# Kernel tuning notes

Hardware: AMD Instinct MI355X
Metric: run time of the kernel (lower is better)

The kernel has to match this reference:

```python
import jax, jax.numpy as jnp
import numpy as np

EPS = 1e-5


def _dwconv(x, w, pad):
    # x: [N,C,H,W]; w: [C,1,k,k] depthwise kernel (groups = C)
    return jax.lax.conv_general_dilated(
        x, w, window_strides=(1, 1), padding=[(pad, pad), (pad, pad)],
        feature_group_count=w.shape[0],
        dimension_numbers=("NCHW", "OIHW", "NCHW"))


def _bn(y, g, b, m, v):
    # inference-mode BatchNorm2d using running stats; per-channel affine
    scale = (g / jnp.sqrt(v + EPS))[None, :, None, None]
    shift = (b - m * g / jnp.sqrt(v + EPS))[None, :, None, None]
    return y * scale + shift


def setup_inputs() -> dict:
    key = jax.random.key(0)
    ks = jax.random.split(key, 16)
    C, KL, KS = 384, 13, 3
    N, H, W = 16, 64, 64
    inp = {
        "x": jax.random.normal(ks[0], (N, C, H, W), jnp.float32),
        "w_large": jax.random.normal(ks[1], (C, 1, KL, KL), jnp.float32) * 0.05,
        "w_small": jax.random.normal(ks[2], (C, 1, KS, KS), jnp.float32) * 0.2,
        "g_l": jax.random.normal(ks[3], (C,), jnp.float32),
        "b_l": jax.random.normal(ks[4], (C,), jnp.float32),
        "m_l": jax.random.normal(ks[5], (C,), jnp.float32),
        "v_l": jax.random.uniform(ks[6], (C,), jnp.float32, 0.5, 1.5),
        "g_s": jax.random.normal(ks[7], (C,), jnp.float32),
        "b_s": jax.random.normal(ks[8], (C,), jnp.float32),
        "m_s": jax.random.normal(ks[9], (C,), jnp.float32),
        "v_s": jax.random.uniform(ks[10], (C,), jnp.float32, 0.5, 1.5),
        "g_i": jax.random.normal(ks[11], (C,), jnp.float32),
        "b_i": jax.random.normal(ks[12], (C,), jnp.float32),
        "m_i": jax.random.normal(ks[13], (C,), jnp.float32),
        "v_i": jax.random.uniform(ks[14], (C,), jnp.float32, 0.5, 1.5),
    }
    return inp


def reference(x, w_large, w_small, g_l, b_l, m_l, v_l,
              g_s, b_s, m_s, v_s, g_i, b_i, m_i, v_i):
    kl = w_large.shape[-1]
    ks = w_small.shape[-1]
    out = (_bn(_dwconv(x, w_large, kl // 2), g_l, b_l, m_l, v_l)
           + _bn(_dwconv(x, w_small, ks // 2), g_s, b_s, m_s, v_s)
           + _bn(x, g_i, b_i, m_i, v_i))
    return out
```

## Files before the change

### kernel.cpp

```cpp
#include <hip/hip_runtime.h>

#define EPSV 1e-5f

typedef __fp16 f16x8 __attribute__((ext_vector_type(8)));
typedef float f32x4 __attribute__((ext_vector_type(4)));
typedef __fp16 half2v __attribute__((ext_vector_type(2)));

__device__ __forceinline__ unsigned h2_as_u32(half2v h) {
    union { half2v h; unsigned u; } cv;
    cv.h = h;
    return cv.u;
}

#define LROWS 76
#define LSTRH 128
#define LSTR32 64

__global__ __launch_bounds__(256) void fuse_weights(
    const float* __restrict__ w_large, const float* __restrict__ w_small,
    const float* __restrict__ g_l, const float* __restrict__ b_l,
    const float* __restrict__ m_l, const float* __restrict__ v_l,
    const float* __restrict__ g_s, const float* __restrict__ b_s,
    const float* __restrict__ m_s, const float* __restrict__ v_s,
    const float* __restrict__ g_i, const float* __restrict__ b_i,
    const float* __restrict__ m_i, const float* __restrict__ v_i,
    float* __restrict__ bf, uint4* __restrict__ wB) {
    __shared__ float sw[169];
    const int c = blockIdx.x;
    const int t = threadIdx.x;
    const float sl = g_l[c] * rsqrtf(v_l[c] + EPSV);
    const float ss = g_s[c] * rsqrtf(v_s[c] + EPSV);
    const float si = g_i[c] * rsqrtf(v_i[c] + EPSV);
    if (t < 169) {
        const int ky = t / 13, kx = t % 13;
        float w = w_large[c * 169 + t] * sl;
        if (ky >= 5 && ky <= 7 && kx >= 5 && kx <= 7)
            w += w_small[c * 9 + (ky - 5) * 3 + (kx - 5)] * ss;
        if (t == 6 * 13 + 6) w += si;
        sw[t] = w;
    }
    if (t == 0)
        bf[c] = (b_l[c] - m_l[c] * sl) + (b_s[c] - m_s[c] * ss) +
                (b_i[c] - m_i[c] * si);
    __syncthreads();
    for (int it = t; it < 832; it += 256) {
        const int dy = it >> 6;
        const int l = it & 63;
        const int i = l & 15;
        const int kb = (l >> 4) * 8;
        unsigned u[4];
#pragma unroll
        for (int jj = 0; jj < 4; ++jj) {
            const int kx0 = kb + 2 * jj - i - 2;
            const int kx1 = kx0 + 1;
            const float w0 =
                (kx0 >= 0 && kx0 <= 12) ? sw[dy * 13 + kx0] : 0.0f;
            const float w1 =
                (kx1 >= 0 && kx1 <= 12) ? sw[dy * 13 + kx1] : 0.0f;
            u[jj] = h2_as_u32(__builtin_amdgcn_cvt_pkrtz(w0, w1));
        }
        wB[(size_t)c * 832 + it] = make_uint4(u[0], u[1], u[2], u[3]);
    }
}

__global__ __launch_bounds__(256, 4) void dwconv_mfma(
    const float* __restrict__ x, const uint4* __restrict__ wB,
    const float* __restrict__ bf, float* __restrict__ out) {
    __shared__ __align__(16) unsigned lds[LROWS * LSTR32];
    __fp16* tile = (__fp16*)lds;

    const int t = threadIdx.x;
    const int img = blockIdx.x;
    const int c = __builtin_amdgcn_readfirstlane(img % 384);
    const size_t base = (size_t)img * 4096;

    const int sr = t >> 2;
    const int sq = t & 3;
    const float4* srcp = (const float4*)(x + base + sr * 64 + sq * 16);
    const float4 xr0 = srcp[0];
    const float4 xr1 = srcp[1];
    const float4 xr2 = srcp[2];
    const float4 xr3 = srcp[3];

    if (t < 192) {
        const int r = t >> 4;
        const int rr = (r < 6) ? r : r + 64;
        *(uint4*)(lds + rr * LSTR32 + (t & 15) * 4) =
            make_uint4(0u, 0u, 0u, 0u);
    }
    if (t < 128) {
        const int r = 6 + (t >> 1);
        const int lc = (t & 1) ? 9 : 0;
        const int pc = lc ^ (r & 7);
        *(uint4*)(lds + r * LSTR32 + pc * 4) = make_uint4(0u, 0u, 0u, 0u);
    }

    {
        const int R = sr + 6;
        unsigned u[8];
        u[0] = h2_as_u32(__builtin_amdgcn_cvt_pkrtz(xr0.x, xr0.y));
        u[1] = h2_as_u32(__builtin_amdgcn_cvt_pkrtz(xr0.z, xr0.w));
        u[2] = h2_as_u32(__builtin_amdgcn_cvt_pkrtz(xr1.x, xr1.y));
        u[3] = h2_as_u32(__builtin_amdgcn_cvt_pkrtz(xr1.z, xr1.w));
        u[4] = h2_as_u32(__builtin_amdgcn_cvt_pkrtz(xr2.x, xr2.y));
        u[5] = h2_as_u32(__builtin_amdgcn_cvt_pkrtz(xr2.z, xr2.w));
        u[6] = h2_as_u32(__builtin_amdgcn_cvt_pkrtz(xr3.x, xr3.y));
        u[7] = h2_as_u32(__builtin_amdgcn_cvt_pkrtz(xr3.z, xr3.w));
        const int p0 = (1 + 2 * sq) ^ (R & 7);
        const int p1 = (2 + 2 * sq) ^ (R & 7);
        *(uint4*)(lds + R * LSTR32 + p0 * 4) = make_uint4(u[0], u[1], u[2], u[3]);
        *(uint4*)(lds + R * LSTR32 + p1 * 4) = make_uint4(u[4], u[5], u[6], u[7]);
    }

    const int l = t & 63;
    const int wv = t >> 6;
    f16x8 Bf[13];
    {
        const uint4* wbp = wB + (size_t)c * 832 + l;
#pragma unroll
        for (int dy = 0; dy < 13; ++dy) {
            union { uint4 u; f16x8 h; } cv;
            cv.u = wbp[dy * 64];
            Bf[dy] = cv.h;
        }
    }
    const float bv = bf[c];

    __syncthreads();

    const int lrow = l & 15;
    const int cb = 2 * wv + (l >> 4);
    f32x4 acc0 = {bv, bv, bv, bv};
    f32x4 acc1 = {bv, bv, bv, bv};
    f32x4 acc2 = {bv, bv, bv, bv};
    f32x4 acc3 = {bv, bv, bv, bv};

#pragma unroll
    for (int dy = 0; dy < 13; ++dy) {
        const int Ra = lrow + dy;
        const int Rb = Ra + 16;
        const int Rc = Ra + 32;
        const int Rd = Ra + 48;
        const f16x8 a0 =
            *(const f16x8*)(tile + (Ra << 7) + ((cb ^ (Ra & 7)) << 3));
        const f16x8 a1 =
            *(const f16x8*)(tile + (Rb << 7) + ((cb ^ (Rb & 7)) << 3));
        const f16x8 a2 =
            *(const f16x8*)(tile + (Rc << 7) + ((cb ^ (Rc & 7)) << 3));
        const f16x8 a3 =
            *(const f16x8*)(tile + (Rd << 7) + ((cb ^ (Rd & 7)) << 3));
        acc0 = __builtin_amdgcn_mfma_f32_16x16x32_f16(a0, Bf[dy], acc0, 0, 0, 0);
        acc1 = __builtin_amdgcn_mfma_f32_16x16x32_f16(a1, Bf[dy], acc1, 0, 0, 0);
        acc2 = __builtin_amdgcn_mfma_f32_16x16x32_f16(a2, Bf[dy], acc2, 0, 0, 0);
        acc3 = __builtin_amdgcn_mfma_f32_16x16x32_f16(a3, Bf[dy], acc3, 0, 0, 0);
    }

    const int ocol = 16 * wv + (l & 15);
    const int orow = 4 * (l >> 4);
    float* ob = out + base;
#pragma unroll
    for (int q = 0; q < 4; ++q) {
        ob[(orow + q) * 64 + ocol] = acc0[q];
        ob[(16 + orow + q) * 64 + ocol] = acc1[q];
        ob[(32 + orow + q) * 64 + ocol] = acc2[q];
        ob[(48 + orow + q) * 64 + ocol] = acc3[q];
    }
}

extern "C" void kernel_launch(void* const* d_in, const int* in_sizes, int n_in,
                              void* d_out, int out_size, void* d_ws,
                              size_t ws_size, hipStream_t stream) {
    const float* x = (const float*)d_in[0];
    const float* w_large = (const float*)d_in[1];
    const float* w_small = (const float*)d_in[2];
    const float* g_l = (const float*)d_in[3];
    const float* b_l = (const float*)d_in[4];
    const float* m_l = (const float*)d_in[5];
    const float* v_l = (const float*)d_in[6];
    const float* g_s = (const float*)d_in[7];
    const float* b_s = (const float*)d_in[8];
    const float* m_s = (const float*)d_in[9];
    const float* v_s = (const float*)d_in[10];
    const float* g_i = (const float*)d_in[11];
    const float* b_i = (const float*)d_in[12];
    const float* m_i = (const float*)d_in[13];
    const float* v_i = (const float*)d_in[14];
    float* outp = (float*)d_out;

    float* bfp = (float*)d_ws;
    uint4* wB = (uint4*)(bfp + 384);

    fuse_weights<<<384, 256, 0, stream>>>(w_large, w_small, g_l, b_l, m_l, v_l,
                                          g_s, b_s, m_s, v_s, g_i, b_i, m_i,
                                          v_i, bfp, wB);
    dwconv_mfma<<<16 * 384, 256, 0, stream>>>(x, wB, bfp, outp);
}
```

Before: 41.98 us.

## Shrink LDS row stride, drop swizzle, split weight loads to raise occupancy

The fp16 LDS tile row stride drops from 128 to 88 halves and the XOR swizzle is removed in favour of padding, which shrinks the per-block shared memory footprint. The 13 per-lane weight fragments are now loaded in two batches (7, then 6 after a sched_barrier), which cuts register pressure. Launch bounds are raised to 6 blocks per CU. The aim is higher occupancy to hide global load latency, at the cost of possible LDS bank conflicts from the unswizzled, padded layout and weight loads that are exposed mid-loop.

```diff
diff --git a/kernel.cpp b/kernel.cpp
--- a/kernel.cpp
+++ b/kernel.cpp
@@ -13,8 +13,8 @@
 }
 
 #define LROWS 76
-#define LSTRH 128
-#define LSTR32 64
+#define LSTRH 88
+#define LSTR32 44
 
 __global__ __launch_bounds__(256) void fuse_weights(
     const float* __restrict__ w_large, const float* __restrict__ w_small,
@@ -63,7 +63,7 @@
     }
 }
 
-__global__ __launch_bounds__(256, 4) void dwconv_mfma(
+__global__ __launch_bounds__(256, 6) void dwconv_mfma(
     const float* __restrict__ x, const uint4* __restrict__ wB,
     const float* __restrict__ bf, float* __restrict__ out) {
     __shared__ __align__(16) unsigned lds[LROWS * LSTR32];
@@ -82,17 +82,17 @@
     const float4 xr2 = srcp[2];
     const float4 xr3 = srcp[3];
 
+    if (t < 132) {
+        const int r = t / 11;
+        const int rr = (r < 6) ? r : r + 64;
+        const int qq = t - r * 11;
+        *(uint4*)(lds + rr * LSTR32 + qq * 4) = make_uint4(0u, 0u, 0u, 0u);
+    }
     if (t < 192) {
-        const int r = t >> 4;
-        const int rr = (r < 6) ? r : r + 64;
-        *(uint4*)(lds + rr * LSTR32 + (t & 15) * 4) =
-            make_uint4(0u, 0u, 0u, 0u);
-    }
-    if (t < 128) {
-        const int r = 6 + (t >> 1);
-        const int lc = (t & 1) ? 9 : 0;
-        const int pc = lc ^ (r & 7);
-        *(uint4*)(lds + r * LSTR32 + pc * 4) = make_uint4(0u, 0u, 0u, 0u);
+        const int r = 6 + t / 3;
+        const int s = t % 3;
+        const int sb = (s == 0) ? 0 : (s == 1 ? 36 : 40);
+        *(uint4*)(lds + r * LSTR32 + sb) = make_uint4(0u, 0u, 0u, 0u);
     }
 
     {
@@ -106,53 +106,66 @@
         u[5] = h2_as_u32(__builtin_amdgcn_cvt_pkrtz(xr2.z, xr2.w));
         u[6] = h2_as_u32(__builtin_amdgcn_cvt_pkrtz(xr3.x, xr3.y));
         u[7] = h2_as_u32(__builtin_amdgcn_cvt_pkrtz(xr3.z, xr3.w));
-        const int p0 = (1 + 2 * sq) ^ (R & 7);
-        const int p1 = (2 + 2 * sq) ^ (R & 7);
-        *(uint4*)(lds + R * LSTR32 + p0 * 4) = make_uint4(u[0], u[1], u[2], u[3]);
-        *(uint4*)(lds + R * LSTR32 + p1 * 4) = make_uint4(u[4], u[5], u[6], u[7]);
+        unsigned* dst = lds + R * LSTR32 + 4 + sq * 8;
+        *(uint4*)dst = make_uint4(u[0], u[1], u[2], u[3]);
+        *(uint4*)(dst + 4) = make_uint4(u[4], u[5], u[6], u[7]);
     }
 
     const int l = t & 63;
     const int wv = t >> 6;
-    f16x8 Bf[13];
-    {
-        const uint4* wbp = wB + (size_t)c * 832 + l;
-#pragma unroll
-        for (int dy = 0; dy < 13; ++dy) {
-            union { uint4 u; f16x8 h; } cv;
-            cv.u = wbp[dy * 64];
-            Bf[dy] = cv.h;
-        }
-    }
+    const uint4* __restrict__ wbp = wB + (size_t)c * 832 + l;
     const float bv = bf[c];
 
+    f16x8 Bf[7];
+#pragma unroll
+    for (int dy = 0; dy < 7; ++dy) {
+        union { uint4 u; f16x8 h; } cv;
+        cv.u = wbp[dy * 64];
+        Bf[dy] = cv.h;
+    }
+
     __syncthreads();
 
     const int lrow = l & 15;
-    const int cb = 2 * wv + (l >> 4);
+    const int kb = (l >> 4) * 8;
+    const __fp16* abase = tile + lrow * LSTRH + 16 * wv + kb;
+
     f32x4 acc0 = {bv, bv, bv, bv};
     f32x4 acc1 = {bv, bv, bv, bv};
     f32x4 acc2 = {bv, bv, bv, bv};
     f32x4 acc3 = {bv, bv, bv, bv};
 
 #pragma unroll
-    for (int dy = 0; dy < 13; ++dy) {
-        const int Ra = lrow + dy;
-        const int Rb = Ra + 16;
-        const int Rc = Ra + 32;
-        const int Rd = Ra + 48;
-        const f16x8 a0 =
-            *(const f16x8*)(tile + (Ra << 7) + ((cb ^ (Ra & 7)) << 3));
-        const f16x8 a1 =
-            *(const f16x8*)(tile + (Rb << 7) + ((cb ^ (Rb & 7)) << 3));
-        const f16x8 a2 =
-            *(const f16x8*)(tile + (Rc << 7) + ((cb ^ (Rc & 7)) << 3));
-        const f16x8 a3 =
-            *(const f16x8*)(tile + (Rd << 7) + ((cb ^ (Rd & 7)) << 3));
+    for (int dy = 0; dy < 7; ++dy) {
+        const f16x8 a0 = *(const f16x8*)(abase + (dy) * LSTRH);
+        const f16x8 a1 = *(const f16x8*)(abase + (16 + dy) * LSTRH);
+        const f16x8 a2 = *(const f16x8*)(abase + (32 + dy) * LSTRH);
+        const f16x8 a3 = *(const f16x8*)(abase + (48 + dy) * LSTRH);
         acc0 = __builtin_amdgcn_mfma_f32_16x16x32_f16(a0, Bf[dy], acc0, 0, 0, 0);
         acc1 = __builtin_amdgcn_mfma_f32_16x16x32_f16(a1, Bf[dy], acc1, 0, 0, 0);
         acc2 = __builtin_amdgcn_mfma_f32_16x16x32_f16(a2, Bf[dy], acc2, 0, 0, 0);
         acc3 = __builtin_amdgcn_mfma_f32_16x16x32_f16(a3, Bf[dy], acc3, 0, 0, 0);
+    }
+
+    __builtin_amdgcn_sched_barrier(0);
+#pragma unroll
+    for (int i = 0; i < 6; ++i) {
+        union { uint4 u; f16x8 h; } cv;
+        cv.u = wbp[(7 + i) * 64];
+        Bf[i] = cv.h;
+    }
+
+#pragma unroll
+    for (int i = 0; i < 6; ++i) {
+        const int dy = 7 + i;
+        const f16x8 a0 = *(const f16x8*)(abase + (dy) * LSTRH);
+        const f16x8 a1 = *(const f16x8*)(abase + (16 + dy) * LSTRH);
+        const f16x8 a2 = *(const f16x8*)(abase + (32 + dy) * LSTRH);
+        const f16x8 a3 = *(const f16x8*)(abase + (48 + dy) * LSTRH);
+        acc0 = __builtin_amdgcn_mfma_f32_16x16x32_f16(a0, Bf[i], acc0, 0, 0, 0);
+        acc1 = __builtin_amdgcn_mfma_f32_16x16x32_f16(a1, Bf[i], acc1, 0, 0, 0);
+        acc2 = __builtin_amdgcn_mfma_f32_16x16x32_f16(a2, Bf[i], acc2, 0, 0, 0);
+        acc3 = __builtin_amdgcn_mfma_f32_16x16x32_f16(a3, Bf[i], acc3, 0, 0, 0);
     }
 
     const int ocol = 16 * wv + (l & 15);
```

After: 107.0 us. 155% more time.
